# Performance work log

Measured on AMD Instinct MI355X. Metric: run time of the kernel, lower is better.

Reference implementation:

```python
import jax, jax.numpy as jnp
import numpy as np

N_NODES = 50000
N_EDGES = 800000
IN_DIM = 256
EMB_DIM = 256
N_COMS = 4
D_COM = EMB_DIM // N_COMS  # 64
BN_EPS = 1e-5


def setup_inputs() -> dict:
    key = jax.random.key(0)
    ks = jax.random.split(key, 16)
    s1 = 1.0 / np.sqrt(IN_DIM)
    s2 = 1.0 / np.sqrt(D_COM)
    return {
        "x": jax.random.normal(ks[0], (N_NODES, IN_DIM), jnp.float32),
        "edge_index": jax.random.randint(ks[1], (2, N_EDGES), 0, N_NODES, jnp.int32),
        "ew": jax.random.uniform(ks[2], (N_COMS, N_EDGES), jnp.float32),
        "W1_0": jax.random.normal(ks[3], (N_COMS, IN_DIM, D_COM), jnp.float32) * s1,
        "b1_0": jnp.zeros((N_COMS, D_COM), jnp.float32),
        "W2_0": jax.random.normal(ks[4], (N_COMS, D_COM, D_COM), jnp.float32) * s2,
        "b2_0": jnp.zeros((N_COMS, D_COM), jnp.float32),
        "g0": jnp.ones((N_COMS, D_COM), jnp.float32),
        "bt0": jnp.zeros((N_COMS, D_COM), jnp.float32),
        "W1_1": jax.random.normal(ks[5], (N_COMS, D_COM, D_COM), jnp.float32) * s2,
        "b1_1": jnp.zeros((N_COMS, D_COM), jnp.float32),
        "W2_1": jax.random.normal(ks[6], (N_COMS, D_COM, D_COM), jnp.float32) * s2,
        "b2_1": jnp.zeros((N_COMS, D_COM), jnp.float32),
        "g1": jnp.ones((N_COMS, D_COM), jnp.float32),
        "bt1": jnp.zeros((N_COMS, D_COM), jnp.float32),
        "encW": jax.random.normal(ks[7], (IN_DIM, EMB_DIM), jnp.float32) * s1,
        "encb": jnp.zeros((EMB_DIM,), jnp.float32),
    }


def _gin_bn_relu(h, src, dst, w, W1, b1, W2, b2, gamma, beta):
    # weighted scatter-add aggregation: agg[i] = sum_{e:(j->i)} w_e * h[j]
    msg = h[src] * w[:, None]                       # [E, F]
    agg = jax.ops.segment_sum(msg, dst, num_segments=N_NODES)
    z = h + agg                                      # eps = 0 (train_eps=False)
    z = jax.nn.relu(z @ W1 + b1) @ W2 + b2           # GIN MLP
    mu = jnp.mean(z, axis=0)
    var = jnp.var(z, axis=0)
    z = gamma * (z - mu) * jax.lax.rsqrt(var + BN_EPS) + beta
    return jax.nn.relu(z)                            # dropout: eval mode no-op


def reference(x, edge_index, ew, W1_0, b1_0, W2_0, b2_0, g0, bt0,
              W1_1, b1_1, W2_1, b2_1, g1, bt1, encW, encb):
    src, dst = edge_index[0], edge_index[1]
    outs1, outs2 = [], []
    for k in range(N_COMS):
        h1 = _gin_bn_relu(x, src, dst, ew[k], W1_0[k], b1_0[k], W2_0[k], b2_0[k], g0[k], bt0[k])
        h2 = _gin_bn_relu(h1, src, dst, ew[k], W1_1[k], b1_1[k], W2_1[k], b2_1[k], g1[k], bt1[k])
        outs1.append(h1)
        outs2.append(h2)
    out1 = jnp.concatenate(outs1, axis=-1)  # [N, emb_dim]
    out2 = jnp.concatenate(outs2, axis=-1)  # [N, emb_dim]
    enc = x @ encW + encb                   # input_encoder
    return (enc, out1, out2)
```

## Files before the change

kernel.cpp:

```cpp
#include <hip/hip_runtime.h>

#define NN 50000
#define NE 800000
#define FDIM 256
#define SCAN_BLOCKS 196

typedef __attribute__((ext_vector_type(8))) short short8v;
typedef __attribute__((ext_vector_type(4))) float float4v;

__device__ __forceinline__ unsigned short f2bf(float f) {
  unsigned u = __float_as_uint(f);
  unsigned r = (u + 0x7fffu + ((u >> 16) & 1u)) >> 16;
  return (unsigned short)r;
}
__device__ __forceinline__ float bf2f(unsigned short b) {
  return __uint_as_float(((unsigned)b) << 16);
}


__global__ __launch_bounds__(256) void k_hist(const int* __restrict__ dst, int* __restrict__ deg) {
  int e = blockIdx.x * 256 + threadIdx.x;
  if (e < NE) atomicAdd(&deg[dst[e]], 1);
}

__device__ __forceinline__ int block_incl_scan(int v, int* wsum) {
  const int tid = threadIdx.x;
  const int lane = tid & 63;
  const int w = tid >> 6;
  int incl = v;
  #pragma unroll
  for (int off = 1; off < 64; off <<= 1) {
    int tmp = __shfl_up(incl, off, 64);
    if (lane >= off) incl += tmp;
  }
  if (lane == 63) wsum[w] = incl;
  __syncthreads();
  int woff = 0;
  #pragma unroll
  for (int k = 0; k < 3; k++)
    if (k < w) woff += wsum[k];
  return woff + incl;
}

__global__ __launch_bounds__(256) void k_scan_a(const int* __restrict__ deg, int* __restrict__ partial) {
  __shared__ int wsum[4];
  int i = blockIdx.x * 256 + threadIdx.x;
  int v = (i < NN) ? deg[i] : 0;
  int incl = block_incl_scan(v, wsum);
  if (threadIdx.x == 255) partial[blockIdx.x] = incl;
}

__global__ __launch_bounds__(256) void k_scanb_wprep(int* __restrict__ partial, int* __restrict__ offs,
                                                     const float* __restrict__ W1_0, const float* __restrict__ encW,
                                                     const float* __restrict__ W1_1, const float* __restrict__ W2_0,
                                                     const float* __restrict__ W2_1, unsigned short* __restrict__ Bt1,
                                                     unsigned short* __restrict__ BtE, unsigned short* __restrict__ Wb11,
                                                     unsigned short* __restrict__ Wb20, unsigned short* __restrict__ Wb21) {
  if (blockIdx.x == 256) {
    __shared__ int wsum[4];
    int tid = threadIdx.x;
    int v = (tid < SCAN_BLOCKS) ? partial[tid] : 0;
    int incl = block_incl_scan(v, wsum);
    if (tid < SCAN_BLOCKS) partial[tid] = incl - v;
    if (tid == 255) offs[NN] = incl;
    return;
  }
  const int t = blockIdx.x;
  const int k = threadIdx.x;
  const int c = t >> 6, j = t & 63;
  Bt1[t * 256 + k] = f2bf(W1_0[c * 16384 + k * 64 + j]);
  BtE[t * 256 + k] = f2bf(encW[k * 256 + t]);
  if (k < 64) {
    Wb11[c * 4096 + j * 64 + k] = f2bf(W1_1[c * 4096 + k * 64 + j]);
    Wb20[c * 4096 + j * 64 + k] = f2bf(W2_0[c * 4096 + k * 64 + j]);
    Wb21[c * 4096 + j * 64 + k] = f2bf(W2_1[c * 4096 + k * 64 + j]);
  }
}

__global__ __launch_bounds__(256) void k_scan_c(const int* __restrict__ deg, const int* __restrict__ partial,
                                                int* __restrict__ offs, int* __restrict__ fillp) {
  __shared__ int wsum[4];
  int i = blockIdx.x * 256 + threadIdx.x;
  int v = (i < NN) ? deg[i] : 0;
  int incl = block_incl_scan(v, wsum);
  int excl = partial[blockIdx.x] + incl - v;
  if (i < NN) {
    offs[i] = excl;
    fillp[i] = excl;
  }
}

__global__ __launch_bounds__(256) void k_fillrec(const int* __restrict__ src, const int* __restrict__ dstA,
                                                 const float* __restrict__ ew, int* __restrict__ fillp,
                                                 int4* __restrict__ recs) {
  int e = blockIdx.x * 256 + threadIdx.x;
  if (e < NE) {
    int d = dstA[e];
    int s = src[e];
    unsigned p01 = (unsigned)f2bf(ew[e]) | ((unsigned)f2bf(ew[NE + e]) << 16);
    unsigned p23 = (unsigned)f2bf(ew[2 * NE + e]) | ((unsigned)f2bf(ew[3 * NE + e]) << 16);
    int pos = atomicAdd(&fillp[d], 1);
    recs[pos] = make_int4(s, (int)p01, (int)p23, 0);
  }
}

__global__ __launch_bounds__(256, 4) void k_mm_fused(const float* __restrict__ x,
                                                     const unsigned short* __restrict__ Bt1,
                                                     const unsigned short* __restrict__ BtE,
                                                     const float* __restrict__ encb,
                                                     unsigned short* __restrict__ Pout,
                                                     float* __restrict__ encout) {
  __shared__ __align__(16) unsigned short xs[64][264];
  const int tid = threadIdx.x;
  const int lane = tid & 63;
  const int w = tid >> 6;
  const int isE = blockIdx.y;
  const int colw = w * 64;
  const int row0 = blockIdx.x * 64;
  const int lr = lane & 15;
  const int lk = (lane >> 4) * 8;
  const int rbase = (lane >> 4) * 4;

  const unsigned short* Bt = isE ? BtE : Bt1;
  const unsigned short* Bptr[4];
  #pragma unroll
  for (int ct = 0; ct < 4; ct++) Bptr[ct] = Bt + (size_t)(colw + ct * 16 + lr) * 256 + lk;

  short8v bcur[4];
  #pragma unroll
  for (int ct = 0; ct < 4; ct++) bcur[ct] = *reinterpret_cast<const short8v*>(Bptr[ct]);

  #pragma unroll
  for (int it = 0; it < 16; it++) {
    int idx = it * 256 + tid;
    int row = idx >> 6;
    int col4 = (idx & 63) * 4;
    int grow = row0 + row;
    if (grow >= NN) grow = NN - 1;
    float4 v = *reinterpret_cast<const float4*>(x + (size_t)grow * 256 + col4);
    ushort4 o;
    o.x = f2bf(v.x); o.y = f2bf(v.y); o.z = f2bf(v.z); o.w = f2bf(v.w);
    *reinterpret_cast<ushort4*>(&xs[row][col4]) = o;
  }
  __syncthreads();

  float4v acc[4][4];
  #pragma unroll
  for (int rt = 0; rt < 4; rt++)
    #pragma unroll
    for (int ct = 0; ct < 4; ct++) acc[rt][ct] = (float4v){0.f, 0.f, 0.f, 0.f};

  #pragma unroll
  for (int ks8 = 0; ks8 < 8; ks8++) {
    const int ks = ks8 * 32;
    short8v bnxt[4];
    if (ks8 < 7) {
      #pragma unroll
      for (int ct = 0; ct < 4; ct++) bnxt[ct] = *reinterpret_cast<const short8v*>(Bptr[ct] + ks + 32);
    }
    short8v a[4];
    #pragma unroll
    for (int rt = 0; rt < 4; rt++)
      a[rt] = *reinterpret_cast<const short8v*>(&xs[rt * 16 + lr][ks + lk]);
    #pragma unroll
    for (int rt = 0; rt < 4; rt++)
      #pragma unroll
      for (int ct = 0; ct < 4; ct++)
        acc[rt][ct] = __builtin_amdgcn_mfma_f32_16x16x32_bf16(a[rt], bcur[ct], acc[rt][ct], 0, 0, 0);
    if (ks8 < 7) {
      #pragma unroll
      for (int ct = 0; ct < 4; ct++) bcur[ct] = bnxt[ct];
    }
  }

  __syncthreads();
  if (!isE) {
    #pragma unroll
    for (int rt = 0; rt < 4; rt++)
      #pragma unroll
      for (int ct = 0; ct < 4; ct++) {
        const int col = colw + ct * 16 + lr;
        #pragma unroll
        for (int r = 0; r < 4; r++) xs[rt * 16 + rbase + r][col] = f2bf(acc[rt][ct][r]);
      }
    __syncthreads();
    #pragma unroll
    for (int it = 0; it < 8; it++) {
      int idx = it * 256 + tid;
      int row = idx >> 5;
      int p = idx & 31;
      if (row0 + row < NN)
        *reinterpret_cast<short8v*>(Pout + (size_t)(row0 + row) * 256 + p * 8) =
            *reinterpret_cast<const short8v*>(&xs[row][p * 8]);
    }
  } else {
    float bv[4];
    #pragma unroll
    for (int ct = 0; ct < 4; ct++) bv[ct] = encb[colw + ct * 16 + lr];
    float (*cs)[132] = reinterpret_cast<float(*)[132]>(&xs[0][0]);
    #pragma unroll
    for (int ph = 0; ph < 2; ph++) {
      if ((colw >> 7) == ph) {
        #pragma unroll
        for (int rt = 0; rt < 4; rt++)
          #pragma unroll
          for (int ct = 0; ct < 4; ct++) {
            const int col = colw + ct * 16 + lr - ph * 128;
            #pragma unroll
            for (int r = 0; r < 4; r++) cs[rt * 16 + rbase + r][col] = acc[rt][ct][r] + bv[ct];
          }
      }
      __syncthreads();
      #pragma unroll
      for (int it = 0; it < 8; it++) {
        int idx = it * 256 + tid;
        int row = idx >> 5;
        int p = idx & 31;
        if (row0 + row < NN)
          *reinterpret_cast<float4*>(encout + (size_t)(row0 + row) * 256 + ph * 128 + p * 4) =
              *reinterpret_cast<const float4*>(&cs[row][p * 4]);
      }
      __syncthreads();
    }
  }
}

__global__ __launch_bounds__(256) void k_agg(const unsigned short* __restrict__ P,
                                             const int* __restrict__ offs, const int4* __restrict__ recs,
                                             const float* __restrict__ b1, unsigned short* __restrict__ Rb) {
  const int lane = threadIdx.x & 63;
  const int wid = threadIdx.x >> 6;
  const int i = blockIdx.x * 4 + wid;
  const int half = lane >> 5;
  const int l32 = lane & 31;
  const int col0 = l32 * 8;
  const int c = l32 >> 3;

  const int es = offs[i], ee = offs[i + 1];
  float acc[8];
  #pragma unroll
  for (int j = 0; j < 8; j++) acc[j] = 0.f;

  for (int base = es; base < ee; base += 16) {
    int sq[8];
    float wq[8];
    #pragma unroll
    for (int q = 0; q < 8; q++) {
      int e = base + 2 * q + half;
      bool valid = e < ee;
      int4 rv = recs[valid ? e : es];
      sq[q] = rv.x;
      unsigned p = (c < 2) ? (unsigned)rv.y : (unsigned)rv.z;
      unsigned short wb = (c & 1) ? (unsigned short)(p >> 16) : (unsigned short)(p & 0xffff);
      wq[q] = valid ? bf2f(wb) : 0.f;
    }
    short8v pq[8];
    #pragma unroll
    for (int q = 0; q < 8; q++)
      pq[q] = *reinterpret_cast<const short8v*>(P + (size_t)sq[q] * 256 + col0);
    #pragma unroll
    for (int q = 0; q < 8; q++)
      #pragma unroll
      for (int j = 0; j < 8; j++)
        acc[j] = fmaf(wq[q], bf2f((unsigned short)pq[q][j]), acc[j]);
  }

  #pragma unroll
  for (int j = 0; j < 8; j++) acc[j] += __shfl_xor(acc[j], 32);

  if (half == 0) {
    short8v ps = *reinterpret_cast<const short8v*>(P + (size_t)i * 256 + col0);
    float4 b4a = *reinterpret_cast<const float4*>(b1 + col0);
    float4 b4b = *reinterpret_cast<const float4*>(b1 + col0 + 4);
    float bb[8] = {b4a.x, b4a.y, b4a.z, b4a.w, b4b.x, b4b.y, b4b.z, b4b.w};
    short8v out;
    #pragma unroll
    for (int j = 0; j < 8; j++) {
      float r = bf2f((unsigned short)ps[j]) + acc[j] + bb[j];
      out[j] = (short)f2bf(r > 0.f ? r : 0.f);
    }
    *reinterpret_cast<short8v*>(Rb + (size_t)i * 256 + col0) = out;
  }
}

__global__ __launch_bounds__(256) void k_bd_stats(const unsigned short* __restrict__ A,
                                                  const unsigned short* __restrict__ Wz,
                                                  float* __restrict__ bnsum, float* __restrict__ bnsq) {
  const int lane = threadIdx.x & 63;
  const int c = threadIdx.x >> 6;
  const int row0 = blockIdx.x * 64;
  const int lr = lane & 15;
  const int lk = (lane >> 4) * 8;

  const unsigned short* Aptr[4];
  #pragma unroll
  for (int rt = 0; rt < 4; rt++) {
    int row = row0 + rt * 16 + lr;
    if (row >= NN) row = NN - 1;
    Aptr[rt] = A + (size_t)row * 256 + c * 64 + lk;
  }

  float4v acc[4][4];
  #pragma unroll
  for (int rt = 0; rt < 4; rt++)
    #pragma unroll
    for (int ct = 0; ct < 4; ct++) acc[rt][ct] = (float4v){0.f, 0.f, 0.f, 0.f};

  #pragma unroll
  for (int ks = 0; ks < 64; ks += 32) {
    short8v a[4], b[4];
    #pragma unroll
    for (int rt = 0; rt < 4; rt++) a[rt] = *reinterpret_cast<const short8v*>(Aptr[rt] + ks);
    #pragma unroll
    for (int ct = 0; ct < 4; ct++)
      b[ct] = *reinterpret_cast<const short8v*>(Wz + (size_t)c * 4096 + (ct * 16 + lr) * 64 + ks + lk);
    #pragma unroll
    for (int rt = 0; rt < 4; rt++)
      #pragma unroll
      for (int ct = 0; ct < 4; ct++)
        acc[rt][ct] = __builtin_amdgcn_mfma_f32_16x16x32_bf16(a[rt], b[ct], acc[rt][ct], 0, 0, 0);
  }

  #pragma unroll
  for (int ct = 0; ct < 4; ct++) {
    const int col = c * 64 + ct * 16 + lr;
    float s1 = 0.f, s2 = 0.f;
    #pragma unroll
    for (int rt = 0; rt < 4; rt++) {
      #pragma unroll
      for (int r = 0; r < 4; r++) {
        const int row = row0 + rt * 16 + (lane >> 4) * 4 + r;
        if (row < NN) {
          float v = acc[rt][ct][r];
          s1 += v;
          s2 += v * v;
        }
      }
    }
    s1 += __shfl_xor(s1, 16); s1 += __shfl_xor(s1, 32);
    s2 += __shfl_xor(s2, 16); s2 += __shfl_xor(s2, 32);
    if (lane < 16) {
      atomicAdd(&bnsum[col], s1);
      atomicAdd(&bnsq[col], s2);
    }
  }
}

template <int WITH_P2>
__global__ __launch_bounds__(256) void k_bd_bn(const unsigned short* __restrict__ A,
                                               const unsigned short* __restrict__ Wz,
                                               const float* __restrict__ bnsum, const float* __restrict__ bnsq,
                                               const float* __restrict__ g, const float* __restrict__ bt,
                                               const unsigned short* __restrict__ Wp,
                                               float* __restrict__ Hout, unsigned short* __restrict__ P2out) {
  __shared__ __align__(16) unsigned short h_lds[64][264];
  const int lane = threadIdx.x & 63;
  const int c = threadIdx.x >> 6;
  const int row0 = blockIdx.x * 64;
  const int lr = lane & 15;
  const int lk = (lane >> 4) * 8;
  const int rbase = (lane >> 4) * 4;

  const unsigned short* Aptr[4];
  #pragma unroll
  for (int rt = 0; rt < 4; rt++) {
    int row = row0 + rt * 16 + lr;
    if (row >= NN) row = NN - 1;
    Aptr[rt] = A + (size_t)row * 256 + c * 64 + lk;
  }

  float4v acc[4][4];
  #pragma unroll
  for (int rt = 0; rt < 4; rt++)
    #pragma unroll
    for (int ct = 0; ct < 4; ct++) acc[rt][ct] = (float4v){0.f, 0.f, 0.f, 0.f};

  #pragma unroll
  for (int ks = 0; ks < 64; ks += 32) {
    short8v a[4], b[4];
    #pragma unroll
    for (int rt = 0; rt < 4; rt++) a[rt] = *reinterpret_cast<const short8v*>(Aptr[rt] + ks);
    #pragma unroll
    for (int ct = 0; ct < 4; ct++)
      b[ct] = *reinterpret_cast<const short8v*>(Wz + (size_t)c * 4096 + (ct * 16 + lr) * 64 + ks + lk);
    #pragma unroll
    for (int rt = 0; rt < 4; rt++)
      #pragma unroll
      for (int ct = 0; ct < 4; ct++)
        acc[rt][ct] = __builtin_amdgcn_mfma_f32_16x16x32_bf16(a[rt], b[ct], acc[rt][ct], 0, 0, 0);
  }

  float sc[4], sh[4];
  #pragma unroll
  for (int ct = 0; ct < 4; ct++) {
    const int t = c * 64 + ct * 16 + lr;
    float mu = bnsum[t] * (1.f / NN);
    float var = bnsq[t] * (1.f / NN) - mu * mu;
    var = var > 0.f ? var : 0.f;
    float rs = rsqrtf(var + 1e-5f);
    sc[ct] = g[t] * rs;
    sh[ct] = bt[t] - mu * sc[ct];
  }

  #pragma unroll
  for (int rt = 0; rt < 4; rt++) {
    #pragma unroll
    for (int ct = 0; ct < 4; ct++) {
      const int col = c * 64 + ct * 16 + lr;
      #pragma unroll
      for (int r = 0; r < 4; r++) {
        const int rowl = rt * 16 + rbase + r;
        const int row = row0 + rowl;
        float h = fmaf(acc[rt][ct][r], sc[ct], sh[ct]);
        h = h > 0.f ? h : 0.f;
        if (row < NN) Hout[(size_t)row * 256 + col] = h;
        if (WITH_P2) h_lds[rowl][col] = f2bf(h);
      }
    }
  }

  if (WITH_P2) {
    __syncthreads();
    float4v acc2[4][4];
    #pragma unroll
    for (int rt = 0; rt < 4; rt++)
      #pragma unroll
      for (int ct = 0; ct < 4; ct++) acc2[rt][ct] = (float4v){0.f, 0.f, 0.f, 0.f};
    #pragma unroll
    for (int ks = 0; ks < 64; ks += 32) {
      short8v a[4], b[4];
      #pragma unroll
      for (int rt = 0; rt < 4; rt++)
        a[rt] = *reinterpret_cast<const short8v*>(&h_lds[rt * 16 + lr][c * 64 + ks + lk]);
      #pragma unroll
      for (int ct = 0; ct < 4; ct++)
        b[ct] = *reinterpret_cast<const short8v*>(Wp + (size_t)c * 4096 + (ct * 16 + lr) * 64 + ks + lk);
      #pragma unroll
      for (int rt = 0; rt < 4; rt++)
        #pragma unroll
        for (int ct = 0; ct < 4; ct++)
          acc2[rt][ct] = __builtin_amdgcn_mfma_f32_16x16x32_bf16(a[rt], b[ct], acc2[rt][ct], 0, 0, 0);
    }
    #pragma unroll
    for (int rt = 0; rt < 4; rt++) {
      #pragma unroll
      for (int ct = 0; ct < 4; ct++) {
        const int col = c * 64 + ct * 16 + lr;
        #pragma unroll
        for (int r = 0; r < 4; r++) {
          const int row = row0 + rt * 16 + rbase + r;
          if (row < NN) P2out[(size_t)row * 256 + col] = f2bf(acc2[rt][ct][r]);
        }
      }
    }
  }
}


extern "C" void kernel_launch(void* const* d_in, const int* in_sizes, int n_in,
                              void* d_out, int out_size, void* d_ws, size_t ws_size,
                              hipStream_t stream) {
  const float* x    = (const float*)d_in[0];
  const int*   ei   = (const int*)d_in[1];
  const float* ew   = (const float*)d_in[2];
  const float* W1_0 = (const float*)d_in[3];
  const float* b1_0 = (const float*)d_in[4];
  const float* W2_0 = (const float*)d_in[5];
  const float* g0   = (const float*)d_in[7];
  const float* bt0  = (const float*)d_in[8];
  const float* W1_1 = (const float*)d_in[9];
  const float* b1_1 = (const float*)d_in[10];
  const float* W2_1 = (const float*)d_in[11];
  const float* g1   = (const float*)d_in[13];
  const float* bt1  = (const float*)d_in[14];
  const float* encW = (const float*)d_in[15];
  const float* encb = (const float*)d_in[16];

  const int* srcA = ei;
  const int* dstA = ei + NE;

  float* out_enc = (float*)d_out;
  float* out1 = out_enc + (size_t)NN * FDIM;
  float* out2 = out1 + (size_t)NN * FDIM;

  unsigned short* P1bf = (unsigned short*)out1;
  unsigned short* P2bf = (unsigned short*)out2;

  char* wp = (char*)d_ws;
  auto carve = [&](size_t bytes) {
    char* r = wp;
    wp += (bytes + 255) & ~(size_t)255;
    return r;
  };
  int*   deg     = (int*)carve((size_t)NN * 4);
  int*   offs    = (int*)carve((size_t)(NN + 1) * 4);
  int*   fillp   = (int*)carve((size_t)NN * 4);
  int*   partial = (int*)carve(SCAN_BLOCKS * 4);
  float* bnsum0  = (float*)carve(256 * 4);
  float* bnsq0   = (float*)carve(256 * 4);
  float* bnsum1  = (float*)carve(256 * 4);
  float* bnsq1   = (float*)carve(256 * 4);
  unsigned short* Bt1  = (unsigned short*)carve(256 * 256 * 2);
  unsigned short* BtE  = (unsigned short*)carve(256 * 256 * 2);
  unsigned short* Wb11 = (unsigned short*)carve(4 * 64 * 64 * 2);
  unsigned short* Wb20 = (unsigned short*)carve(4 * 64 * 64 * 2);
  unsigned short* Wb21 = (unsigned short*)carve(4 * 64 * 64 * 2);
  int4* recs           = (int4*)carve((size_t)NE * 16);
  unsigned short* Rb   = (unsigned short*)carve((size_t)NN * FDIM * 2);

  hipMemsetAsync(deg, 0, (size_t)NN * 4, stream);
  hipMemsetAsync(bnsum0, 0, 4 * 1024, stream);

  k_hist<<<(NE + 255) / 256, 256, 0, stream>>>(dstA, deg);
  k_scan_a<<<SCAN_BLOCKS, 256, 0, stream>>>(deg, partial);
  k_scanb_wprep<<<257, 256, 0, stream>>>(partial, offs, W1_0, encW, W1_1, W2_0, W2_1,
                                         Bt1, BtE, Wb11, Wb20, Wb21);
  k_scan_c<<<SCAN_BLOCKS, 256, 0, stream>>>(deg, partial, offs, fillp);
  k_fillrec<<<(NE + 255) / 256, 256, 0, stream>>>(srcA, dstA, ew, fillp, recs);

  const int MMG = (NN + 63) / 64;

  k_mm_fused<<<dim3(MMG, 2), 256, 0, stream>>>(x, Bt1, BtE, encb, P1bf, out_enc);

  k_agg<<<NN / 4, 256, 0, stream>>>(P1bf, offs, recs, b1_0, Rb);
  k_bd_stats<<<MMG, 256, 0, stream>>>(Rb, Wb20, bnsum0, bnsq0);
  k_bd_bn<1><<<MMG, 256, 0, stream>>>(Rb, Wb20, bnsum0, bnsq0, g0, bt0, Wb11, out1, P2bf);

  k_agg<<<NN / 4, 256, 0, stream>>>(P2bf, offs, recs, b1_1, Rb);
  k_bd_stats<<<MMG, 256, 0, stream>>>(Rb, Wb21, bnsum1, bnsq1);
  k_bd_bn<0><<<MMG, 256, 0, stream>>>(Rb, Wb21, bnsum1, bnsq1, g1, bt1, nullptr, out2, nullptr);
}
```

Measured before the change: 384.1 us.

## Merge edge fill with input matmul and assign one node per half-wave in aggregation

The edge-record fill kernel and the dual input matmul become one launch, with a block-index split, so the atomic scatter and the GEMM blocks can run at the same time and one launch is removed. The aggregation kernel now gives each 32-lane half-wave its own destination node and walks 16 edges per step, instead of two half-waves splitting one node's edges and combining them with a shuffle. This removes the cross-half reduction and halves the grid. The price is more imbalance between half-waves on nodes of different degree and more registers held for 16 in-flight gathers.

```diff
diff --git a/kernel.cpp b/kernel.cpp
--- a/kernel.cpp
+++ b/kernel.cpp
@@ -4,6 +4,8 @@
 #define NE 800000
 #define FDIM 256
 #define SCAN_BLOCKS 196
+#define FILL_BLOCKS 3125
+#define MMG 782
 
 typedef __attribute__((ext_vector_type(8))) short short8v;
 typedef __attribute__((ext_vector_type(4))) float float4v;
@@ -90,33 +92,35 @@
   }
 }
 
-__global__ __launch_bounds__(256) void k_fillrec(const int* __restrict__ src, const int* __restrict__ dstA,
-                                                 const float* __restrict__ ew, int* __restrict__ fillp,
-                                                 int4* __restrict__ recs) {
-  int e = blockIdx.x * 256 + threadIdx.x;
-  if (e < NE) {
+__global__ __launch_bounds__(256, 4) void k_fill_mm(const int* __restrict__ src, const int* __restrict__ dstA,
+                                                    const float* __restrict__ ew, int* __restrict__ fillp,
+                                                    int4* __restrict__ recs, const float* __restrict__ x,
+                                                    const unsigned short* __restrict__ Bt1,
+                                                    const unsigned short* __restrict__ BtE,
+                                                    const float* __restrict__ encb,
+                                                    unsigned short* __restrict__ Pout,
+                                                    float* __restrict__ encout) {
+  __shared__ __align__(16) unsigned short xs[64][264];
+  const int tid = threadIdx.x;
+
+  if (blockIdx.x < FILL_BLOCKS) {
+    int e = blockIdx.x * 256 + tid;
     int d = dstA[e];
     int s = src[e];
     unsigned p01 = (unsigned)f2bf(ew[e]) | ((unsigned)f2bf(ew[NE + e]) << 16);
     unsigned p23 = (unsigned)f2bf(ew[2 * NE + e]) | ((unsigned)f2bf(ew[3 * NE + e]) << 16);
     int pos = atomicAdd(&fillp[d], 1);
     recs[pos] = make_int4(s, (int)p01, (int)p23, 0);
-  }
-}
-
-__global__ __launch_bounds__(256, 4) void k_mm_fused(const float* __restrict__ x,
-                                                     const unsigned short* __restrict__ Bt1,
-                                                     const unsigned short* __restrict__ BtE,
-                                                     const float* __restrict__ encb,
-                                                     unsigned short* __restrict__ Pout,
-                                                     float* __restrict__ encout) {
-  __shared__ __align__(16) unsigned short xs[64][264];
-  const int tid = threadIdx.x;
+    return;
+  }
+
+  const int bx = blockIdx.x - FILL_BLOCKS;
+  const int isE = bx >= MMG;
+  const int bm = isE ? bx - MMG : bx;
   const int lane = tid & 63;
   const int w = tid >> 6;
-  const int isE = blockIdx.y;
   const int colw = w * 64;
-  const int row0 = blockIdx.x * 64;
+  const int row0 = bm * 64;
   const int lr = lane & 15;
   const int lk = (lane >> 4) * 8;
   const int rbase = (lane >> 4) * 4;
@@ -230,8 +234,8 @@
                                              const float* __restrict__ b1, unsigned short* __restrict__ Rb) {
   const int lane = threadIdx.x & 63;
   const int wid = threadIdx.x >> 6;
-  const int i = blockIdx.x * 4 + wid;
   const int half = lane >> 5;
+  const int i = blockIdx.x * 8 + wid * 2 + half;
   const int l32 = lane & 31;
   const int col0 = l32 * 8;
   const int c = l32 >> 3;
@@ -242,45 +246,40 @@
   for (int j = 0; j < 8; j++) acc[j] = 0.f;
 
   for (int base = es; base < ee; base += 16) {
-    int sq[8];
-    float wq[8];
-    #pragma unroll
-    for (int q = 0; q < 8; q++) {
-      int e = base + 2 * q + half;
+    int sq[16];
+    float wq[16];
+    #pragma unroll
+    for (int q = 0; q < 16; q++) {
+      int e = base + q;
       bool valid = e < ee;
       int4 rv = recs[valid ? e : es];
-      sq[q] = rv.x;
+      sq[q] = valid ? rv.x : 0;
       unsigned p = (c < 2) ? (unsigned)rv.y : (unsigned)rv.z;
       unsigned short wb = (c & 1) ? (unsigned short)(p >> 16) : (unsigned short)(p & 0xffff);
       wq[q] = valid ? bf2f(wb) : 0.f;
     }
-    short8v pq[8];
-    #pragma unroll
-    for (int q = 0; q < 8; q++)
+    short8v pq[16];
+    #pragma unroll
+    for (int q = 0; q < 16; q++)
       pq[q] = *reinterpret_cast<const short8v*>(P + (size_t)sq[q] * 256 + col0);
     #pragma unroll
-    for (int q = 0; q < 8; q++)
+    for (int q = 0; q < 16; q++)
       #pragma unroll
       for (int j = 0; j < 8; j++)
         acc[j] = fmaf(wq[q], bf2f((unsigned short)pq[q][j]), acc[j]);
   }
 
-  #pragma unroll
-  for (int j = 0; j < 8; j++) acc[j] += __shfl_xor(acc[j], 32);
-
-  if (half == 0) {
-    short8v ps = *reinterpret_cast<const short8v*>(P + (size_t)i * 256 + col0);
-    float4 b4a = *reinterpret_cast<const float4*>(b1 + col0);
-    float4 b4b = *reinterpret_cast<const float4*>(b1 + col0 + 4);
-    float bb[8] = {b4a.x, b4a.y, b4a.z, b4a.w, b4b.x, b4b.y, b4b.z, b4b.w};
-    short8v out;
-    #pragma unroll
-    for (int j = 0; j < 8; j++) {
-      float r = bf2f((unsigned short)ps[j]) + acc[j] + bb[j];
-      out[j] = (short)f2bf(r > 0.f ? r : 0.f);
-    }
-    *reinterpret_cast<short8v*>(Rb + (size_t)i * 256 + col0) = out;
-  }
+  short8v ps = *reinterpret_cast<const short8v*>(P + (size_t)i * 256 + col0);
+  float4 b4a = *reinterpret_cast<const float4*>(b1 + col0);
+  float4 b4b = *reinterpret_cast<const float4*>(b1 + col0 + 4);
+  float bb[8] = {b4a.x, b4a.y, b4a.z, b4a.w, b4b.x, b4b.y, b4b.z, b4b.w};
+  short8v out;
+  #pragma unroll
+  for (int j = 0; j < 8; j++) {
+    float r = bf2f((unsigned short)ps[j]) + acc[j] + bb[j];
+    out[j] = (short)f2bf(r > 0.f ? r : 0.f);
+  }
+  *reinterpret_cast<short8v*>(Rb + (size_t)i * 256 + col0) = out;
 }
 
 __global__ __launch_bounds__(256) void k_bd_stats(const unsigned short* __restrict__ A,
@@ -516,17 +515,15 @@
   k_scanb_wprep<<<257, 256, 0, stream>>>(partial, offs, W1_0, encW, W1_1, W2_0, W2_1,
                                          Bt1, BtE, Wb11, Wb20, Wb21);
   k_scan_c<<<SCAN_BLOCKS, 256, 0, stream>>>(deg, partial, offs, fillp);
-  k_fillrec<<<(NE + 255) / 256, 256, 0, stream>>>(srcA, dstA, ew, fillp, recs);
-
-  const int MMG = (NN + 63) / 64;
-
-  k_mm_fused<<<dim3(MMG, 2), 256, 0, stream>>>(x, Bt1, BtE, encb, P1bf, out_enc);
-
-  k_agg<<<NN / 4, 256, 0, stream>>>(P1bf, offs, recs, b1_0, Rb);
+
+  k_fill_mm<<<FILL_BLOCKS + 2 * MMG, 256, 0, stream>>>(srcA, dstA, ew, fillp, recs,
+                                                       x, Bt1, BtE, encb, P1bf, out_enc);
+
+  k_agg<<<NN / 8, 256, 0, stream>>>(P1bf, offs, recs, b1_0, Rb);
   k_bd_stats<<<MMG, 256, 0, stream>>>(Rb, Wb20, bnsum0, bnsq0);
   k_bd_bn<1><<<MMG, 256, 0, stream>>>(Rb, Wb20, bnsum0, bnsq0, g0, bt0, Wb11, out1, P2bf);
 
-  k_agg<<<NN / 4, 256, 0, stream>>>(P2bf, offs, recs, b1_1, Rb);
+  k_agg<<<NN / 8, 256, 0, stream>>>(P2bf, offs, recs, b1_1, Rb);
   k_bd_stats<<<MMG, 256, 0, stream>>>(Rb, Wb21, bnsum1, bnsq1);
   k_bd_bn<0><<<MMG, 256, 0, stream>>>(Rb, Wb21, bnsum1, bnsq1, g1, bt1, nullptr, out2, nullptr);
 }
```

After: 405.7 us. 5.6% more time.

## Fuse edge-record fill into the input GEMM kernel and halve row tile

Applied to the files above, without the earlier changes.

Merges the CSR record-fill pass (atomic slot claim plus packed bf16 weights) into the x@W GEMM kernel. Each of the 2x1563 blocks handles one 256-edge chunk alongside a 32-row GEMM tile, which removes one launch and overlaps the scattered atomics and writes with the GEMM loads. The row tile drops from 64 to 32, so there are twice as many blocks and each does less MFMA work, but every block reloads the B fragments. The x loads are issued into registers before conversion, and the two memsets are merged into one by putting the BN buffers next to deg.

```diff
diff --git a/kernel.cpp b/kernel.cpp
--- a/kernel.cpp
+++ b/kernel.cpp
@@ -4,6 +4,8 @@
 #define NE 800000
 #define FDIM 256
 #define SCAN_BLOCKS 196
+#define MMG 782
+#define G32 1563
 
 typedef __attribute__((ext_vector_type(8))) short short8v;
 typedef __attribute__((ext_vector_type(4))) float float4v;
@@ -90,37 +92,33 @@
   }
 }
 
-__global__ __launch_bounds__(256) void k_fillrec(const int* __restrict__ src, const int* __restrict__ dstA,
+__global__ __launch_bounds__(256) void k_fill_mm(const float* __restrict__ x,
+                                                 const unsigned short* __restrict__ Bt1,
+                                                 const unsigned short* __restrict__ BtE,
+                                                 const float* __restrict__ encb,
+                                                 const int* __restrict__ srcA, const int* __restrict__ dstA,
                                                  const float* __restrict__ ew, int* __restrict__ fillp,
-                                                 int4* __restrict__ recs) {
-  int e = blockIdx.x * 256 + threadIdx.x;
-  if (e < NE) {
-    int d = dstA[e];
-    int s = src[e];
-    unsigned p01 = (unsigned)f2bf(ew[e]) | ((unsigned)f2bf(ew[NE + e]) << 16);
-    unsigned p23 = (unsigned)f2bf(ew[2 * NE + e]) | ((unsigned)f2bf(ew[3 * NE + e]) << 16);
-    int pos = atomicAdd(&fillp[d], 1);
-    recs[pos] = make_int4(s, (int)p01, (int)p23, 0);
-  }
-}
-
-__global__ __launch_bounds__(256, 4) void k_mm_fused(const float* __restrict__ x,
-                                                     const unsigned short* __restrict__ Bt1,
-                                                     const unsigned short* __restrict__ BtE,
-                                                     const float* __restrict__ encb,
-                                                     unsigned short* __restrict__ Pout,
-                                                     float* __restrict__ encout) {
-  __shared__ __align__(16) unsigned short xs[64][264];
+                                                 int4* __restrict__ recs,
+                                                 unsigned short* __restrict__ Pout,
+                                                 float* __restrict__ encout) {
+  __shared__ __align__(16) unsigned short xs[32][264];
   const int tid = threadIdx.x;
   const int lane = tid & 63;
   const int w = tid >> 6;
   const int isE = blockIdx.y;
   const int colw = w * 64;
-  const int row0 = blockIdx.x * 64;
+  const int row0 = blockIdx.x * 32;
   const int lr = lane & 15;
   const int lk = (lane >> 4) * 8;
   const int rbase = (lane >> 4) * 4;
 
+  const int e = (isE * G32 + blockIdx.x) * 256 + tid;
+  const bool ev = e < NE;
+  const int ec = ev ? e : 0;
+  int sA = srcA[ec];
+  int dA = dstA[ec];
+  float w0 = ew[ec], w1 = ew[NE + ec], w2 = ew[2 * NE + ec], w3 = ew[3 * NE + ec];
+
   const unsigned short* Bt = isE ? BtE : Bt1;
   const unsigned short* Bptr[4];
   #pragma unroll
@@ -130,23 +128,33 @@
   #pragma unroll
   for (int ct = 0; ct < 4; ct++) bcur[ct] = *reinterpret_cast<const short8v*>(Bptr[ct]);
 
-  #pragma unroll
-  for (int it = 0; it < 16; it++) {
+  float4 xv[8];
+  #pragma unroll
+  for (int it = 0; it < 8; it++) {
     int idx = it * 256 + tid;
-    int row = idx >> 6;
-    int col4 = (idx & 63) * 4;
-    int grow = row0 + row;
+    int grow = row0 + (idx >> 6);
     if (grow >= NN) grow = NN - 1;
-    float4 v = *reinterpret_cast<const float4*>(x + (size_t)grow * 256 + col4);
+    xv[it] = *reinterpret_cast<const float4*>(x + (size_t)grow * 256 + (idx & 63) * 4);
+  }
+  #pragma unroll
+  for (int it = 0; it < 8; it++) {
+    int idx = it * 256 + tid;
     ushort4 o;
-    o.x = f2bf(v.x); o.y = f2bf(v.y); o.z = f2bf(v.z); o.w = f2bf(v.w);
-    *reinterpret_cast<ushort4*>(&xs[row][col4]) = o;
+    o.x = f2bf(xv[it].x); o.y = f2bf(xv[it].y); o.z = f2bf(xv[it].z); o.w = f2bf(xv[it].w);
+    *reinterpret_cast<ushort4*>(&xs[idx >> 6][(idx & 63) * 4]) = o;
+  }
+
+  if (ev) {
+    unsigned p01 = (unsigned)f2bf(w0) | ((unsigned)f2bf(w1) << 16);
+    unsigned p23 = (unsigned)f2bf(w2) | ((unsigned)f2bf(w3) << 16);
+    int pos = atomicAdd(&fillp[dA], 1);
+    recs[pos] = make_int4(sA, (int)p01, (int)p23, 0);
   }
   __syncthreads();
 
-  float4v acc[4][4];
-  #pragma unroll
-  for (int rt = 0; rt < 4; rt++)
+  float4v acc[2][4];
+  #pragma unroll
+  for (int rt = 0; rt < 2; rt++)
     #pragma unroll
     for (int ct = 0; ct < 4; ct++) acc[rt][ct] = (float4v){0.f, 0.f, 0.f, 0.f};
 
@@ -158,12 +166,12 @@
       #pragma unroll
       for (int ct = 0; ct < 4; ct++) bnxt[ct] = *reinterpret_cast<const short8v*>(Bptr[ct] + ks + 32);
     }
-    short8v a[4];
-    #pragma unroll
-    for (int rt = 0; rt < 4; rt++)
+    short8v a[2];
+    #pragma unroll
+    for (int rt = 0; rt < 2; rt++)
       a[rt] = *reinterpret_cast<const short8v*>(&xs[rt * 16 + lr][ks + lk]);
     #pragma unroll
-    for (int rt = 0; rt < 4; rt++)
+    for (int rt = 0; rt < 2; rt++)
       #pragma unroll
       for (int ct = 0; ct < 4; ct++)
         acc[rt][ct] = __builtin_amdgcn_mfma_f32_16x16x32_bf16(a[rt], bcur[ct], acc[rt][ct], 0, 0, 0);
@@ -176,7 +184,7 @@
   __syncthreads();
   if (!isE) {
     #pragma unroll
-    for (int rt = 0; rt < 4; rt++)
+    for (int rt = 0; rt < 2; rt++)
       #pragma unroll
       for (int ct = 0; ct < 4; ct++) {
         const int col = colw + ct * 16 + lr;
@@ -185,7 +193,7 @@
       }
     __syncthreads();
     #pragma unroll
-    for (int it = 0; it < 8; it++) {
+    for (int it = 0; it < 4; it++) {
       int idx = it * 256 + tid;
       int row = idx >> 5;
       int p = idx & 31;
@@ -202,7 +210,7 @@
     for (int ph = 0; ph < 2; ph++) {
       if ((colw >> 7) == ph) {
         #pragma unroll
-        for (int rt = 0; rt < 4; rt++)
+        for (int rt = 0; rt < 2; rt++)
           #pragma unroll
           for (int ct = 0; ct < 4; ct++) {
             const int col = colw + ct * 16 + lr - ph * 128;
@@ -212,7 +220,7 @@
       }
       __syncthreads();
       #pragma unroll
-      for (int it = 0; it < 8; it++) {
+      for (int it = 0; it < 4; it++) {
         int idx = it * 256 + tid;
         int row = idx >> 5;
         int p = idx & 31;
@@ -493,13 +501,13 @@
     return r;
   };
   int*   deg     = (int*)carve((size_t)NN * 4);
-  int*   offs    = (int*)carve((size_t)(NN + 1) * 4);
-  int*   fillp   = (int*)carve((size_t)NN * 4);
-  int*   partial = (int*)carve(SCAN_BLOCKS * 4);
   float* bnsum0  = (float*)carve(256 * 4);
   float* bnsq0   = (float*)carve(256 * 4);
   float* bnsum1  = (float*)carve(256 * 4);
   float* bnsq1   = (float*)carve(256 * 4);
+  int*   offs    = (int*)carve((size_t)(NN + 1) * 4);
+  int*   fillp   = (int*)carve((size_t)NN * 4);
+  int*   partial = (int*)carve(SCAN_BLOCKS * 4);
   unsigned short* Bt1  = (unsigned short*)carve(256 * 256 * 2);
   unsigned short* BtE  = (unsigned short*)carve(256 * 256 * 2);
   unsigned short* Wb11 = (unsigned short*)carve(4 * 64 * 64 * 2);
@@ -508,19 +516,17 @@
   int4* recs           = (int4*)carve((size_t)NE * 16);
   unsigned short* Rb   = (unsigned short*)carve((size_t)NN * FDIM * 2);
 
-  hipMemsetAsync(deg, 0, (size_t)NN * 4, stream);
-  hipMemsetAsync(bnsum0, 0, 4 * 1024, stream);
+  const size_t zspan = (((size_t)NN * 4 + 255) & ~(size_t)255) + 4 * 1024;
+  hipMemsetAsync(deg, 0, zspan, stream);
 
   k_hist<<<(NE + 255) / 256, 256, 0, stream>>>(dstA, deg);
   k_scan_a<<<SCAN_BLOCKS, 256, 0, stream>>>(deg, partial);
   k_scanb_wprep<<<257, 256, 0, stream>>>(partial, offs, W1_0, encW, W1_1, W2_0, W2_1,
                                          Bt1, BtE, Wb11, Wb20, Wb21);
   k_scan_c<<<SCAN_BLOCKS, 256, 0, stream>>>(deg, partial, offs, fillp);
-  k_fillrec<<<(NE + 255) / 256, 256, 0, stream>>>(srcA, dstA, ew, fillp, recs);
-
-  const int MMG = (NN + 63) / 64;
-
-  k_mm_fused<<<dim3(MMG, 2), 256, 0, stream>>>(x, Bt1, BtE, encb, P1bf, out_enc);
+
+  k_fill_mm<<<dim3(G32, 2), 256, 0, stream>>>(x, Bt1, BtE, encb, srcA, dstA, ew, fillp, recs,
+                                              P1bf, out_enc);
 
   k_agg<<<NN / 4, 256, 0, stream>>>(P1bf, offs, recs, b1_0, Rb);
   k_bd_stats<<<MMG, 256, 0, stream>>>(Rb, Wb20, bnsum0, bnsq0);
```

After: 356.7 us. 1.08x faster.
